# Optimization experiments

Measured on AMD Instinct MI355X. Metric: run time of the kernel, lower is better.

Reference implementation:

```python
import jax, jax.numpy as jnp
import numpy as np

DIM = 4096
N_HEADS = 32
N_KV_HEADS = 8
HEAD_DIM = DIM // N_HEADS
N_REP = N_HEADS // N_KV_HEADS
SEQ_LEN = 2048
ROPE_THETA = 10000.0


def rope_cos_sin(head_dim, seq_len, theta):
    freqs = 1.0 / (theta ** (jnp.arange(0, head_dim, 2, dtype=jnp.float32) / head_dim))  # [hd/2]
    t = jnp.arange(seq_len, dtype=jnp.float32)
    angles = jnp.outer(t, freqs)  # [S, hd/2]
    return jnp.cos(angles), jnp.sin(angles)


def apply_rope(x, cos, sin):
    # x: [B, S, H, hd]; complex rotation on interleaved (even, odd) pairs
    xr = x[..., 0::2].astype(jnp.float32)
    xi = x[..., 1::2].astype(jnp.float32)
    c = cos[None, :, None, :]
    s = sin[None, :, None, :]
    out_r = xr * c - xi * s
    out_i = xr * s + xi * c
    out = jnp.stack([out_r, out_i], axis=-1).reshape(x.shape)
    return out.astype(x.dtype)


def setup_inputs() -> dict:
    key = jax.random.key(0)
    ks = jax.random.split(key, 5)
    x = jax.random.normal(ks[0], (1, SEQ_LEN, DIM), dtype=jnp.float32)
    wq = jax.random.normal(ks[1], (DIM, DIM), dtype=jnp.float32) * (DIM ** -0.5)
    wk = jax.random.normal(ks[2], (N_KV_HEADS * HEAD_DIM, DIM), dtype=jnp.float32) * (DIM ** -0.5)
    wv = jax.random.normal(ks[3], (N_KV_HEADS * HEAD_DIM, DIM), dtype=jnp.float32) * (DIM ** -0.5)
    wo = jax.random.normal(ks[4], (DIM, DIM), dtype=jnp.float32) * (DIM ** -0.5)
    return {"x": x, "start_pos": 0, "wq": wq, "wk": wk, "wv": wv, "wo": wo}


def reference(x, start_pos, wq, wk, wv, wo):
    bsz, seq_len, _ = x.shape
    # projections (torch Linear: y = x @ W.T)
    xq = (x @ wq.T).reshape(bsz, seq_len, N_HEADS, HEAD_DIM)
    xk = (x @ wk.T).reshape(bsz, seq_len, N_KV_HEADS, HEAD_DIM)
    xv = (x @ wv.T).reshape(bsz, seq_len, N_KV_HEADS, HEAD_DIM)

    cos, sin = rope_cos_sin(HEAD_DIM, seq_len, ROPE_THETA)
    xq = apply_rope(xq, cos, sin)
    xk = apply_rope(xk, cos, sin)

    # repeat_kv (GQA): [B, S, Hkv, hd] -> [B, S, Hkv*n_rep, hd]
    keys = jnp.repeat(xk, N_REP, axis=2)
    values = jnp.repeat(xv, N_REP, axis=2)

    # [B, H, S, hd]
    q = xq.transpose(0, 2, 1, 3)
    k = keys.transpose(0, 2, 1, 3)
    v = values.transpose(0, 2, 1, 3)

    scale = 1.0 / jnp.sqrt(jnp.asarray(HEAD_DIM, dtype=jnp.float32))
    scores = jnp.einsum('bhqd,bhkd->bhqk', q, k) * scale  # [B, H, S, S]
    causal = jnp.tril(jnp.ones((seq_len, seq_len), dtype=bool))
    scores = jnp.where(causal[None, None], scores, -jnp.inf)
    attn = jax.nn.softmax(scores.astype(jnp.float32), axis=-1).astype(q.dtype)
    out = jnp.einsum('bhqk,bhkd->bhqd', attn, v)  # [B, H, S, hd]
    out = out.transpose(0, 2, 1, 3).reshape(bsz, seq_len, -1)
    return out @ wo.T
```

## Files before the change

kernel.cpp:

```cpp
#include <hip/hip_runtime.h>

#define DIM 4096
#define KVDIM 1024
#define KVSTRIDE 2048
#define SEQ 2048
#define HEADS 32
#define HD 128

typedef __attribute__((ext_vector_type(8))) short bf16x8;
typedef __attribute__((ext_vector_type(4))) float f32x4;
typedef __attribute__((ext_vector_type(16))) float f32x16;
typedef __attribute__((ext_vector_type(4))) int int4v;

__device__ inline unsigned short f2bf(float f) {
    union { float f; unsigned int u; } v; v.f = f;
    unsigned int r = v.u + 0x7fffu + ((v.u >> 16) & 1u);
    return (unsigned short)(r >> 16);
}
__device__ inline float bf2f(unsigned short h) {
    union { unsigned int u; float f; } v; v.u = ((unsigned int)h) << 16;
    return v.f;
}

__device__ inline void gld16(const void* g, void* l) {
    __builtin_amdgcn_global_load_lds(
        (const __attribute__((address_space(1))) void*)g,
        (__attribute__((address_space(3))) void*)l, 16, 0, 0);
}

__device__ inline unsigned cvtpk(float a, float b) {
    unsigned r;
    asm("v_cvt_pk_bf16_f32 %0, %1, %2" : "=v"(r) : "v"(a), "v"(b));
    return r;
}

__global__ void convert_f32_bf16(const float* __restrict__ in,
                                 unsigned short* __restrict__ out, int n) {
    int i = (blockIdx.x * blockDim.x + threadIdx.x) * 8;
    if (i >= n) return;
    const float4* p = (const float4*)(in + i);
    float4 a = p[0], b = p[1];
    bf16x8 o;
    o[0] = (short)f2bf(a.x); o[1] = (short)f2bf(a.y);
    o[2] = (short)f2bf(a.z); o[3] = (short)f2bf(a.w);
    o[4] = (short)f2bf(b.x); o[5] = (short)f2bf(b.y);
    o[6] = (short)f2bf(b.z); o[7] = (short)f2bf(b.w);
    *(bf16x8*)(out + i) = o;
}

__global__ void rope_table(float* __restrict__ cs, float* __restrict__ sn) {
    int i = blockIdx.x * blockDim.x + threadIdx.x;
    if (i >= SEQ * 64) return;
    int m = i >> 6, f = i & 63;
    float freq = expf(-(float)f * (9.210340371976184f / 64.0f));
    float ang = (float)m * freq;
    float s, c;
    sincosf(ang, &s, &c);
    cs[i] = c; sn[i] = s;
}

__global__ void rope_apply(unsigned short* __restrict__ q, int lppr, int stride, float scale,
                           const float* __restrict__ cs, const float* __restrict__ sn) {
    int i = blockIdx.x * blockDim.x + threadIdx.x;
    int m = i >> lppr;
    int p = i & ((1 << lppr) - 1);
    if (m >= SEQ) return;
    int f = p & 63;
    int col = ((p >> 6) << 7) + (f << 1);
    size_t idx = (size_t)m * stride + col;
    unsigned int u = *(const unsigned int*)&q[idx];
    float xr = bf2f((unsigned short)(u & 0xffffu));
    float xi = bf2f((unsigned short)(u >> 16));
    float c = cs[(m << 6) + f], s = sn[(m << 6) + f];
    float orr = (xr * c - xi * s) * scale;
    float oi  = (xr * s + xi * c) * scale;
    unsigned int w = ((unsigned int)f2bf(oi) << 16) | (unsigned int)f2bf(orr);
    *(unsigned int*)&q[idx] = w;
}

template <bool OUT_BF16>
__global__ __launch_bounds__(256)
void gemm_bt(const unsigned short* __restrict__ A,
             const unsigned short* __restrict__ W,
             void* __restrict__ Cout, int M, int N, int K) {
    __shared__ __align__(16) unsigned short As[128 * 64];
    __shared__ __align__(16) unsigned short Ws[128 * 64];

    int nwg = gridDim.x * gridDim.y;
    int wg = blockIdx.y * gridDim.x + blockIdx.x;
    int cpx = nwg >> 3;
    wg = (wg & 7) * cpx + (wg >> 3);
    int bx = wg % gridDim.x, by = wg / gridDim.x;
    int brow = by * 128, bcol = bx * 128;

    int tid = threadIdx.x, lane = tid & 63, wid = tid >> 6;
    int wr = wid >> 1, wc = wid & 1, l15 = lane & 15, lq = lane >> 4;

    f32x4 acc[4][4] = {};

    for (int bk = 0; bk < K; bk += 64) {
        #pragma unroll
        for (int it = 0; it < 4; ++it) {
            int slot = it * 256 + wid * 64 + lane;
            int r = slot >> 3, g = slot & 7;
            gld16(&A[(size_t)(brow + r) * K + bk + ((g ^ (r & 7)) << 3)],
                  &As[(it * 256 + wid * 64) * 8]);
        }
        #pragma unroll
        for (int it = 0; it < 4; ++it) {
            int slot = it * 256 + wid * 64 + lane;
            int r = slot >> 3, g = slot & 7;
            gld16(&W[(size_t)(bcol + r) * K + bk + ((g ^ (r & 7)) << 3)],
                  &Ws[(it * 256 + wid * 64) * 8]);
        }
        __syncthreads();

        #pragma unroll
        for (int kk = 0; kk < 64; kk += 32) {
            int gb = (kk >> 3) + lq;
            bf16x8 af[4], bfr[4];
            #pragma unroll
            for (int m = 0; m < 4; ++m) {
                int r = wr * 64 + m * 16 + l15;
                af[m] = *(const bf16x8*)&As[r * 64 + ((gb ^ (r & 7)) << 3)];
            }
            #pragma unroll
            for (int n = 0; n < 4; ++n) {
                int r = wc * 64 + n * 16 + l15;
                bfr[n] = *(const bf16x8*)&Ws[r * 64 + ((gb ^ (r & 7)) << 3)];
            }
            #pragma unroll
            for (int m = 0; m < 4; ++m)
                #pragma unroll
                for (int n = 0; n < 4; ++n)
                    acc[m][n] = __builtin_amdgcn_mfma_f32_16x16x32_bf16(
                        af[m], bfr[n], acc[m][n], 0, 0, 0);
        }
        __syncthreads();
    }

    #pragma unroll
    for (int m = 0; m < 4; ++m) {
        #pragma unroll
        for (int n = 0; n < 4; ++n) {
            int row0 = brow + wr * 64 + m * 16 + lq * 4;
            int col = bcol + wc * 64 + n * 16 + l15;
            #pragma unroll
            for (int r = 0; r < 4; ++r) {
                if (OUT_BF16)
                    ((unsigned short*)Cout)[(size_t)(row0 + r) * N + col] = f2bf(acc[m][n][r]);
                else
                    ((float*)Cout)[(size_t)(row0 + r) * N + col] = acc[m][n][r];
            }
        }
    }
}

__global__ __launch_bounds__(256)
void attn_kernel(const unsigned short* __restrict__ Q,
                 const unsigned short* __restrict__ KV,
                 unsigned short* __restrict__ O) {
    __shared__ __align__(16) unsigned short ks[2][64 * 128];
    __shared__ __align__(16) unsigned short vt[2][128][66];

    int h = blockIdx.x;
    int yy = (gridDim.y - 1) - blockIdx.y;
    int q0 = yy * 128;
    int kvh = h >> 2;
    int tid = threadIdx.x, lane = tid & 63, wid = tid >> 6;
    int l31 = lane & 31, l5 = lane >> 5;
    int qw0 = q0 + wid * 32;

    bf16x8 qf[8];
    #pragma unroll
    for (int k8 = 0; k8 < 8; ++k8)
        qf[k8] = *(const bf16x8*)&Q[(size_t)(qw0 + l31) * DIM + h * HD + k8 * 16 + l5 * 8];

    f32x16 o_acc[4] = {};
    float m_run = -1e30f, l_run = 0.0f;

    int k4 = tid >> 4;
    int d0 = (tid & 15) * 8;

    const unsigned short* Kbase = KV + kvh * HD;
    const unsigned short* Vbase = KV + KVDIM + kvh * HD;

    int ntiles = (q0 + 128) >> 6;
    bf16x8 vr[4];

    #pragma unroll
    for (int it = 0; it < 4; ++it) {
        int slot = it * 256 + wid * 64 + lane;
        int r = slot >> 4, g = slot & 15;
        gld16(&Kbase[(size_t)r * KVSTRIDE + ((g ^ (r & 7)) << 3)],
              &ks[0][(it * 256 + wid * 64) * 8]);
    }
    #pragma unroll
    for (int j = 0; j < 4; ++j)
        vr[j] = *(const bf16x8*)&Vbase[(size_t)(k4 * 4 + j) * KVSTRIDE + d0];
    asm volatile("s_waitcnt vmcnt(0)" ::: "memory");
    #pragma unroll
    for (int j = 0; j < 8; ++j) {
        unsigned lo = ((unsigned)(unsigned short)vr[1][j] << 16) | (unsigned)(unsigned short)vr[0][j];
        unsigned hi = ((unsigned)(unsigned short)vr[3][j] << 16) | (unsigned)(unsigned short)vr[2][j];
        *(unsigned*)&vt[0][d0 + j][k4 * 4]     = lo;
        *(unsigned*)&vt[0][d0 + j][k4 * 4 + 2] = hi;
    }
    __syncthreads();

    for (int t = 0; t < ntiles; ++t) {
        int b = t & 1;
        int kv0 = t * 64;
        bool pre = (t + 1 < ntiles);
        if (pre) {
            int kvn = kv0 + 64;
            #pragma unroll
            for (int it = 0; it < 4; ++it) {
                int slot = it * 256 + wid * 64 + lane;
                int r = slot >> 4, g = slot & 15;
                gld16(&Kbase[(size_t)(kvn + r) * KVSTRIDE + ((g ^ (r & 7)) << 3)],
                      &ks[b ^ 1][(it * 256 + wid * 64) * 8]);
            }
            #pragma unroll
            for (int j = 0; j < 4; ++j)
                vr[j] = *(const bf16x8*)&Vbase[(size_t)(kvn + k4 * 4 + j) * KVSTRIDE + d0];
        }

        if (kv0 <= qw0 + 31) {
            #pragma unroll
            for (int sub = 0; sub < 2; ++sub) {
                int kvs = kv0 + sub * 32;
                if (kvs > qw0 + 31) continue;
                f32x16 s = {};
                __builtin_amdgcn_s_setprio(1);
                #pragma unroll
                for (int k8 = 0; k8 < 8; ++k8) {
                    int r = sub * 32 + l31;
                    bf16x8 kf = *(const bf16x8*)&ks[b][r * 128 + (((k8 * 2 + l5) ^ (r & 7)) << 3)];
                    s = __builtin_amdgcn_mfma_f32_32x32x16_bf16(kf, qf[k8], s, 0, 0, 0);
                }
                __builtin_amdgcn_s_setprio(0);
                if (kvs + 31 > qw0) {
                    #pragma unroll
                    for (int r = 0; r < 16; ++r) {
                        int kv = kvs + (r & 3) + ((r >> 2) << 3) + l5 * 4;
                        if (kv > qw0 + l31) s[r] = -1e30f;
                    }
                }
                float mx = s[0];
                #pragma unroll
                for (int r = 1; r < 16; ++r) mx = fmaxf(mx, s[r]);
                mx = fmaxf(mx, __shfl_xor(mx, 32));
                bool need = mx > m_run + 8.0f;
                if (__any((int)need)) {
                    float mn = fmaxf(m_run, mx);
                    float al = exp2f(m_run - mn);
                    m_run = mn;
                    l_run *= al;
                    #pragma unroll
                    for (int r = 0; r < 16; ++r) {
                        int qlr = (r & 3) + ((r >> 2) << 3) + l5 * 4;
                        float alO = __shfl(al, qlr, 32);
                        #pragma unroll
                        for (int t32 = 0; t32 < 4; ++t32) o_acc[t32][r] *= alO;
                    }
                }
                #pragma unroll
                for (int r = 0; r < 16; ++r) {
                    float p = exp2f(s[r] - m_run);
                    l_run += p;
                    s[r] = p;
                }
                bf16x8 pa[2];
                #pragma unroll
                for (int kk1 = 0; kk1 < 2; ++kk1) {
                    unsigned u0 = cvtpk(s[kk1 * 8 + 0], s[kk1 * 8 + 1]);
                    unsigned u1 = cvtpk(s[kk1 * 8 + 2], s[kk1 * 8 + 3]);
                    unsigned u2 = cvtpk(s[kk1 * 8 + 4], s[kk1 * 8 + 5]);
                    unsigned u3 = cvtpk(s[kk1 * 8 + 6], s[kk1 * 8 + 7]);
                    unsigned t0 = (unsigned)__shfl_xor((int)(l5 ? u0 : u2), 32);
                    unsigned t1 = (unsigned)__shfl_xor((int)(l5 ? u1 : u3), 32);
                    int4v w;
                    w.x = (int)(l5 ? t0 : u0);
                    w.y = (int)(l5 ? t1 : u1);
                    w.z = (int)(l5 ? u2 : t0);
                    w.w = (int)(l5 ? u3 : t1);
                    pa[kk1] = __builtin_bit_cast(bf16x8, w);
                }
                __builtin_amdgcn_s_setprio(1);
                #pragma unroll
                for (int t32 = 0; t32 < 4; ++t32) {
                    #pragma unroll
                    for (int kk1 = 0; kk1 < 2; ++kk1) {
                        const unsigned short* vrow =
                            &vt[b][t32 * 32 + l31][sub * 32 + kk1 * 16 + l5 * 8];
                        int4v w;
                        w.x = *(const int*)&vrow[0];
                        w.y = *(const int*)&vrow[2];
                        w.z = *(const int*)&vrow[4];
                        w.w = *(const int*)&vrow[6];
                        o_acc[t32] = __builtin_amdgcn_mfma_f32_32x32x16_bf16(
                            pa[kk1], __builtin_bit_cast(bf16x8, w), o_acc[t32], 0, 0, 0);
                    }
                }
                __builtin_amdgcn_s_setprio(0);
            }
        }

        if (pre) {
            asm volatile("s_waitcnt vmcnt(0)" ::: "memory");
            #pragma unroll
            for (int j = 0; j < 8; ++j) {
                unsigned lo = ((unsigned)(unsigned short)vr[1][j] << 16) | (unsigned)(unsigned short)vr[0][j];
                unsigned hi = ((unsigned)(unsigned short)vr[3][j] << 16) | (unsigned)(unsigned short)vr[2][j];
                *(unsigned*)&vt[b ^ 1][d0 + j][k4 * 4]     = lo;
                *(unsigned*)&vt[b ^ 1][d0 + j][k4 * 4 + 2] = hi;
            }
        }
        __syncthreads();
    }

    float l_tot = l_run + __shfl_xor(l_run, 32);
    float rinv = __builtin_amdgcn_rcpf(l_tot);
    #pragma unroll
    for (int r = 0; r < 16; ++r) {
        int qlr = (r & 3) + ((r >> 2) << 3) + l5 * 4;
        float rl = __shfl(rinv, qlr, 32);
        #pragma unroll
        for (int t32 = 0; t32 < 4; ++t32)
            O[(size_t)(qw0 + qlr) * DIM + h * HD + t32 * 32 + l31] =
                f2bf(o_acc[t32][r] * rl);
    }
}

extern "C" void kernel_launch(void* const* d_in, const int* in_sizes, int n_in,
                              void* d_out, int out_size, void* d_ws, size_t ws_size,
                              hipStream_t stream) {
    const float* x  = (const float*)d_in[0];
    const float* wq = (const float*)d_in[2];
    const float* wk = (const float*)d_in[3];
    const float* wv = (const float*)d_in[4];
    const float* wo = (const float*)d_in[5];
    float* out = (float*)d_out;

    char* ws = (char*)d_ws;
    unsigned short* xb  = (unsigned short*)(ws);
    unsigned short* qb  = (unsigned short*)(ws + 16777216);
    unsigned short* kvb = (unsigned short*)(ws + 33554432);
    unsigned short* ab  = (unsigned short*)(ws + 41943040);
    float* cs = (float*)(ws + 58720256);
    float* sn = cs + SEQ * 64;
    unsigned short* wscratch = (unsigned short*)d_out;
    unsigned short* wob = (unsigned short*)(ws);

    const float SCALE2 = 0.08838834764831845f * 1.4426950408889634f;

    convert_f32_bf16<<<SEQ * DIM / 2048, 256, 0, stream>>>(x, xb, SEQ * DIM);
    rope_table<<<SEQ * 64 / 256, 256, 0, stream>>>(cs, sn);

    convert_f32_bf16<<<DIM * DIM / 2048, 256, 0, stream>>>(wq, wscratch, DIM * DIM);
    gemm_bt<true><<<dim3(DIM / 128, SEQ / 128), 256, 0, stream>>>(xb, wscratch, qb, SEQ, DIM, DIM);

    convert_f32_bf16<<<KVDIM * DIM / 2048, 256, 0, stream>>>(wk, wscratch, KVDIM * DIM);
    convert_f32_bf16<<<KVDIM * DIM / 2048, 256, 0, stream>>>(wv, wscratch + (size_t)KVDIM * DIM, KVDIM * DIM);
    gemm_bt<true><<<dim3(KVSTRIDE / 128, SEQ / 128), 256, 0, stream>>>(xb, wscratch, kvb, SEQ, KVSTRIDE, DIM);

    rope_apply<<<SEQ * (DIM / 2) / 256, 256, 0, stream>>>(qb, 11, DIM, SCALE2, cs, sn);
    rope_apply<<<SEQ * (KVDIM / 2) / 256, 256, 0, stream>>>(kvb, 9, KVSTRIDE, 1.0f, cs, sn);

    attn_kernel<<<dim3(HEADS, SEQ / 128), 256, 0, stream>>>(qb, kvb, ab);

    convert_f32_bf16<<<DIM * DIM / 2048, 256, 0, stream>>>(wo, wob, DIM * DIM);
    gemm_bt<false><<<dim3(DIM / 128, SEQ / 128), 256, 0, stream>>>(ab, wob, out, SEQ, DIM, DIM);
}
```

Measured before the change: 401.6 us.

## Pair causal query tiles per attention block and swizzle V-transpose LDS layout

Each attention block now handles two 128-row query tiles, a short one (yy) and a long one (15-yy). It streams the K/V tiles once, sharing each K/V load and LDS fragment between both tiles and keeping two sets of online-softmax state. This balances causal work across blocks and halves the grid to 256 blocks. The padded V-transpose buffer is also replaced by an XOR-swizzled unpadded layout, so V fragments load as single 16-byte LDS reads. In exchange it doubles the Q/accumulator register footprint, which may lower occupancy, and on MI355X's 256 CUs the smaller grid gives roughly one block per CU.

```diff
diff --git a/kernel.cpp b/kernel.cpp
--- a/kernel.cpp
+++ b/kernel.cpp
@@ -11,6 +11,7 @@
 typedef __attribute__((ext_vector_type(4))) float f32x4;
 typedef __attribute__((ext_vector_type(16))) float f32x16;
 typedef __attribute__((ext_vector_type(4))) int int4v;
+typedef __attribute__((ext_vector_type(2))) unsigned int u32x2;
 
 __device__ inline unsigned short f2bf(float f) {
     union { float f; unsigned int u; } v; v.f = f;
@@ -156,37 +157,96 @@
     }
 }
 
+
+__device__ __forceinline__ void softmax_pack(
+    f32x16& s, f32x16* o_acc, float& m_run, float& l_run,
+    int qw0, int kvs, int l31, int l5, bf16x8* pa) {
+    if (kvs + 31 > qw0) {
+        #pragma unroll
+        for (int r = 0; r < 16; ++r) {
+            int kv = kvs + (r & 3) + ((r >> 2) << 3) + l5 * 4;
+            if (kv > qw0 + l31) s[r] = -1e30f;
+        }
+    }
+    float mx = s[0];
+    #pragma unroll
+    for (int r = 1; r < 16; ++r) mx = fmaxf(mx, s[r]);
+    mx = fmaxf(mx, __shfl_xor(mx, 32));
+    bool need = mx > m_run + 8.0f;
+    if (__any((int)need)) {
+        float mn = fmaxf(m_run, mx);
+        float al = exp2f(m_run - mn);
+        m_run = mn;
+        l_run *= al;
+        #pragma unroll
+        for (int r = 0; r < 16; ++r) {
+            int qlr = (r & 3) + ((r >> 2) << 3) + l5 * 4;
+            float alO = __shfl(al, qlr, 32);
+            #pragma unroll
+            for (int t32 = 0; t32 < 4; ++t32) o_acc[t32][r] *= alO;
+        }
+    }
+    #pragma unroll
+    for (int r = 0; r < 16; ++r) {
+        float p = exp2f(s[r] - m_run);
+        l_run += p;
+        s[r] = p;
+    }
+    #pragma unroll
+    for (int kk1 = 0; kk1 < 2; ++kk1) {
+        unsigned u0 = cvtpk(s[kk1 * 8 + 0], s[kk1 * 8 + 1]);
+        unsigned u1 = cvtpk(s[kk1 * 8 + 2], s[kk1 * 8 + 3]);
+        unsigned u2 = cvtpk(s[kk1 * 8 + 4], s[kk1 * 8 + 5]);
+        unsigned u3 = cvtpk(s[kk1 * 8 + 6], s[kk1 * 8 + 7]);
+        unsigned t0 = (unsigned)__shfl_xor((int)(l5 ? u0 : u2), 32);
+        unsigned t1 = (unsigned)__shfl_xor((int)(l5 ? u1 : u3), 32);
+        int4v w;
+        w.x = (int)(l5 ? t0 : u0);
+        w.y = (int)(l5 ? t1 : u1);
+        w.z = (int)(l5 ? u2 : t0);
+        w.w = (int)(l5 ? u3 : t1);
+        pa[kk1] = __builtin_bit_cast(bf16x8, w);
+    }
+}
+
 __global__ __launch_bounds__(256)
 void attn_kernel(const unsigned short* __restrict__ Q,
                  const unsigned short* __restrict__ KV,
                  unsigned short* __restrict__ O) {
     __shared__ __align__(16) unsigned short ks[2][64 * 128];
-    __shared__ __align__(16) unsigned short vt[2][128][66];
+    __shared__ __align__(16) unsigned short vt[2][128 * 64];
 
     int h = blockIdx.x;
-    int yy = (gridDim.y - 1) - blockIdx.y;
-    int q0 = yy * 128;
+    int yy = blockIdx.y;
+    int q0A = yy * 128;
+    int q0B = (15 - yy) * 128;
     int kvh = h >> 2;
     int tid = threadIdx.x, lane = tid & 63, wid = tid >> 6;
     int l31 = lane & 31, l5 = lane >> 5;
-    int qw0 = q0 + wid * 32;
-
-    bf16x8 qf[8];
-    #pragma unroll
-    for (int k8 = 0; k8 < 8; ++k8)
-        qf[k8] = *(const bf16x8*)&Q[(size_t)(qw0 + l31) * DIM + h * HD + k8 * 16 + l5 * 8];
-
-    f32x16 o_acc[4] = {};
-    float m_run = -1e30f, l_run = 0.0f;
+    int qwA = q0A + wid * 32;
+    int qwB = q0B + wid * 32;
+
+    bf16x8 qfA[8], qfB[8];
+    #pragma unroll
+    for (int k8 = 0; k8 < 8; ++k8) {
+        qfA[k8] = *(const bf16x8*)&Q[(size_t)(qwA + l31) * DIM + h * HD + k8 * 16 + l5 * 8];
+        qfB[k8] = *(const bf16x8*)&Q[(size_t)(qwB + l31) * DIM + h * HD + k8 * 16 + l5 * 8];
+    }
+
+    f32x16 oA[4] = {}, oB[4] = {};
+    float mA = -1e30f, lA = 0.0f, mB = -1e30f, lB = 0.0f;
 
     int k4 = tid >> 4;
     int d0 = (tid & 15) * 8;
+    int vhalf = (k4 & 1) * 4;
+    int vgran = k4 >> 1;
 
     const unsigned short* Kbase = KV + kvh * HD;
     const unsigned short* Vbase = KV + KVDIM + kvh * HD;
 
-    int ntiles = (q0 + 128) >> 6;
+    int ntiles = (q0B + 128) >> 6;
     bf16x8 vr[4];
+
 
     #pragma unroll
     for (int it = 0; it < 4; ++it) {
@@ -201,10 +261,12 @@
     asm volatile("s_waitcnt vmcnt(0)" ::: "memory");
     #pragma unroll
     for (int j = 0; j < 8; ++j) {
-        unsigned lo = ((unsigned)(unsigned short)vr[1][j] << 16) | (unsigned)(unsigned short)vr[0][j];
-        unsigned hi = ((unsigned)(unsigned short)vr[3][j] << 16) | (unsigned)(unsigned short)vr[2][j];
-        *(unsigned*)&vt[0][d0 + j][k4 * 4]     = lo;
-        *(unsigned*)&vt[0][d0 + j][k4 * 4 + 2] = hi;
+        int row = d0 + j;
+        int g2 = (vgran ^ (((row >> 3) ^ row) & 7)) << 3;
+        u32x2 w;
+        w.x = ((unsigned)(unsigned short)vr[1][j] << 16) | (unsigned)(unsigned short)vr[0][j];
+        w.y = ((unsigned)(unsigned short)vr[3][j] << 16) | (unsigned)(unsigned short)vr[2][j];
+        *(u32x2*)&vt[0][row * 64 + g2 + vhalf] = w;
     }
     __syncthreads();
 
@@ -226,110 +288,76 @@
                 vr[j] = *(const bf16x8*)&Vbase[(size_t)(kvn + k4 * 4 + j) * KVSTRIDE + d0];
         }
 
-        if (kv0 <= qw0 + 31) {
-            #pragma unroll
-            for (int sub = 0; sub < 2; ++sub) {
-                int kvs = kv0 + sub * 32;
-                if (kvs > qw0 + 31) continue;
-                f32x16 s = {};
-                __builtin_amdgcn_s_setprio(1);
-                #pragma unroll
-                for (int k8 = 0; k8 < 8; ++k8) {
-                    int r = sub * 32 + l31;
-                    bf16x8 kf = *(const bf16x8*)&ks[b][r * 128 + (((k8 * 2 + l5) ^ (r & 7)) << 3)];
-                    s = __builtin_amdgcn_mfma_f32_32x32x16_bf16(kf, qf[k8], s, 0, 0, 0);
-                }
-                __builtin_amdgcn_s_setprio(0);
-                if (kvs + 31 > qw0) {
-                    #pragma unroll
-                    for (int r = 0; r < 16; ++r) {
-                        int kv = kvs + (r & 3) + ((r >> 2) << 3) + l5 * 4;
-                        if (kv > qw0 + l31) s[r] = -1e30f;
-                    }
-                }
-                float mx = s[0];
-                #pragma unroll
-                for (int r = 1; r < 16; ++r) mx = fmaxf(mx, s[r]);
-                mx = fmaxf(mx, __shfl_xor(mx, 32));
-                bool need = mx > m_run + 8.0f;
-                if (__any((int)need)) {
-                    float mn = fmaxf(m_run, mx);
-                    float al = exp2f(m_run - mn);
-                    m_run = mn;
-                    l_run *= al;
-                    #pragma unroll
-                    for (int r = 0; r < 16; ++r) {
-                        int qlr = (r & 3) + ((r >> 2) << 3) + l5 * 4;
-                        float alO = __shfl(al, qlr, 32);
-                        #pragma unroll
-                        for (int t32 = 0; t32 < 4; ++t32) o_acc[t32][r] *= alO;
-                    }
-                }
-                #pragma unroll
-                for (int r = 0; r < 16; ++r) {
-                    float p = exp2f(s[r] - m_run);
-                    l_run += p;
-                    s[r] = p;
-                }
-                bf16x8 pa[2];
+        #pragma unroll
+        for (int sub = 0; sub < 2; ++sub) {
+            int kvs = kv0 + sub * 32;
+            bool actA = (kvs <= qwA + 31);
+            bool actB = (kvs <= qwB + 31);
+            if (!actA && !actB) continue;
+
+            f32x16 sA = {}, sB = {};
+            __builtin_amdgcn_s_setprio(1);
+            #pragma unroll
+            for (int k8 = 0; k8 < 8; ++k8) {
+                int r = sub * 32 + l31;
+                bf16x8 kf = *(const bf16x8*)&ks[b][r * 128 + (((k8 * 2 + l5) ^ (r & 7)) << 3)];
+                if (actA) sA = __builtin_amdgcn_mfma_f32_32x32x16_bf16(kf, qfA[k8], sA, 0, 0, 0);
+                if (actB) sB = __builtin_amdgcn_mfma_f32_32x32x16_bf16(kf, qfB[k8], sB, 0, 0, 0);
+            }
+            __builtin_amdgcn_s_setprio(0);
+
+            bf16x8 paA[2], paB[2];
+            if (actA) softmax_pack(sA, oA, mA, lA, qwA, kvs, l31, l5, paA);
+            if (actB) softmax_pack(sB, oB, mB, lB, qwB, kvs, l31, l5, paB);
+
+            __builtin_amdgcn_s_setprio(1);
+            #pragma unroll
+            for (int t32 = 0; t32 < 4; ++t32) {
+                int d = t32 * 32 + l31;
+                int swz = ((d >> 3) ^ d) & 7;
                 #pragma unroll
                 for (int kk1 = 0; kk1 < 2; ++kk1) {
-                    unsigned u0 = cvtpk(s[kk1 * 8 + 0], s[kk1 * 8 + 1]);
-                    unsigned u1 = cvtpk(s[kk1 * 8 + 2], s[kk1 * 8 + 3]);
-                    unsigned u2 = cvtpk(s[kk1 * 8 + 4], s[kk1 * 8 + 5]);
-                    unsigned u3 = cvtpk(s[kk1 * 8 + 6], s[kk1 * 8 + 7]);
-                    unsigned t0 = (unsigned)__shfl_xor((int)(l5 ? u0 : u2), 32);
-                    unsigned t1 = (unsigned)__shfl_xor((int)(l5 ? u1 : u3), 32);
-                    int4v w;
-                    w.x = (int)(l5 ? t0 : u0);
-                    w.y = (int)(l5 ? t1 : u1);
-                    w.z = (int)(l5 ? u2 : t0);
-                    w.w = (int)(l5 ? u3 : t1);
-                    pa[kk1] = __builtin_bit_cast(bf16x8, w);
+                    int g = sub * 4 + kk1 * 2 + l5;
+                    int4v w = *(const int4v*)&vt[b][d * 64 + ((g ^ swz) << 3)];
+                    bf16x8 vf = __builtin_bit_cast(bf16x8, w);
+                    if (actA) oA[t32] = __builtin_amdgcn_mfma_f32_32x32x16_bf16(paA[kk1], vf, oA[t32], 0, 0, 0);
+                    if (actB) oB[t32] = __builtin_amdgcn_mfma_f32_32x32x16_bf16(paB[kk1], vf, oB[t32], 0, 0, 0);
                 }
-                __builtin_amdgcn_s_setprio(1);
-                #pragma unroll
-                for (int t32 = 0; t32 < 4; ++t32) {
-                    #pragma unroll
-                    for (int kk1 = 0; kk1 < 2; ++kk1) {
-                        const unsigned short* vrow =
-                            &vt[b][t32 * 32 + l31][sub * 32 + kk1 * 16 + l5 * 8];
-                        int4v w;
-                        w.x = *(const int*)&vrow[0];
-                        w.y = *(const int*)&vrow[2];
-                        w.z = *(const int*)&vrow[4];
-                        w.w = *(const int*)&vrow[6];
-                        o_acc[t32] = __builtin_amdgcn_mfma_f32_32x32x16_bf16(
-                            pa[kk1], __builtin_bit_cast(bf16x8, w), o_acc[t32], 0, 0, 0);
-                    }
-                }
-                __builtin_amdgcn_s_setprio(0);
-            }
+            }
+            __builtin_amdgcn_s_setprio(0);
         }
 
         if (pre) {
             asm volatile("s_waitcnt vmcnt(0)" ::: "memory");
             #pragma unroll
             for (int j = 0; j < 8; ++j) {
-                unsigned lo = ((unsigned)(unsigned short)vr[1][j] << 16) | (unsigned)(unsigned short)vr[0][j];
-                unsigned hi = ((unsigned)(unsigned short)vr[3][j] << 16) | (unsigned)(unsigned short)vr[2][j];
-                *(unsigned*)&vt[b ^ 1][d0 + j][k4 * 4]     = lo;
-                *(unsigned*)&vt[b ^ 1][d0 + j][k4 * 4 + 2] = hi;
+                int row = d0 + j;
+                int g2 = (vgran ^ (((row >> 3) ^ row) & 7)) << 3;
+                u32x2 w;
+                w.x = ((unsigned)(unsigned short)vr[1][j] << 16) | (unsigned)(unsigned short)vr[0][j];
+                w.y = ((unsigned)(unsigned short)vr[3][j] << 16) | (unsigned)(unsigned short)vr[2][j];
+                *(u32x2*)&vt[b ^ 1][row * 64 + g2 + vhalf] = w;
             }
         }
         __syncthreads();
     }
 
-    float l_tot = l_run + __shfl_xor(l_run, 32);
-    float rinv = __builtin_amdgcn_rcpf(l_tot);
-    #pragma unroll
-    for (int r = 0; r < 16; ++r) {
-        int qlr = (r & 3) + ((r >> 2) << 3) + l5 * 4;
-        float rl = __shfl(rinv, qlr, 32);
-        #pragma unroll
-        for (int t32 = 0; t32 < 4; ++t32)
-            O[(size_t)(qw0 + qlr) * DIM + h * HD + t32 * 32 + l31] =
-                f2bf(o_acc[t32][r] * rl);
+    #pragma unroll
+    for (int side = 0; side < 2; ++side) {
+        f32x16* oo = side ? oB : oA;
+        float lr = side ? lB : lA;
+        int qw = side ? qwB : qwA;
+        float l_tot = lr + __shfl_xor(lr, 32);
+        float rinv = __builtin_amdgcn_rcpf(l_tot);
+        #pragma unroll
+        for (int r = 0; r < 16; ++r) {
+            int qlr = (r & 3) + ((r >> 2) << 3) + l5 * 4;
+            float rl = __shfl(rinv, qlr, 32);
+            #pragma unroll
+            for (int t32 = 0; t32 < 4; ++t32)
+                O[(size_t)(qw + qlr) * DIM + h * HD + t32 * 32 + l31] =
+                    f2bf(oo[t32][r] * rl);
+        }
     }
 }
 
@@ -368,7 +396,7 @@
     rope_apply<<<SEQ * (DIM / 2) / 256, 256, 0, stream>>>(qb, 11, DIM, SCALE2, cs, sn);
     rope_apply<<<SEQ * (KVDIM / 2) / 256, 256, 0, stream>>>(kvb, 9, KVSTRIDE, 1.0f, cs, sn);
 
-    attn_kernel<<<dim3(HEADS, SEQ / 128), 256, 0, stream>>>(qb, kvb, ab);
+    attn_kernel<<<dim3(HEADS, 8), 256, 0, stream>>>(qb, kvb, ab);
 
     convert_f32_bf16<<<DIM * DIM / 2048, 256, 0, stream>>>(wo, wob, DIM * DIM);
     gemm_bt<false><<<dim3(DIM / 128, SEQ / 128), 256, 0, stream>>>(ab, wob, out, SEQ, DIM, DIM);
```

Measured after the change: 439.8 us. 9.5% more time.
